# Performance work log

Hardware: AMD Instinct MI355X
Metric: run time of the kernel (lower is better)

## Reference

```python
import jax, jax.numpy as jnp
import numpy as np

D_IN = 1024
D_OUT = 1024
NUM_HEADS = 16
HEAD_DIM = D_OUT // NUM_HEADS


def setup_inputs() -> dict:
    key = jax.random.key(0)
    ks = jax.random.split(key, 6)
    B, T = 2, 2048
    x = jax.random.normal(ks[0], (B, T, D_IN), dtype=jnp.float32)
    s = 1.0 / np.sqrt(D_IN)
    Wq = jax.random.normal(ks[1], (D_IN, D_OUT), dtype=jnp.float32) * s
    Wk = jax.random.normal(ks[2], (D_IN, D_OUT), dtype=jnp.float32) * s
    Wv = jax.random.normal(ks[3], (D_IN, D_OUT), dtype=jnp.float32) * s
    Wo = jax.random.normal(ks[4], (D_OUT, D_OUT), dtype=jnp.float32) * (1.0 / np.sqrt(D_OUT))
    bo = jnp.zeros((D_OUT,), dtype=jnp.float32)
    return {"x": x, "Wq": Wq, "Wk": Wk, "Wv": Wv, "Wo": Wo, "bo": bo}


def reference(x, Wq, Wk, Wv, Wo, bo):
    B, T, _ = x.shape
    # project and split heads -> (B, H, T, Dh)
    def split(t):
        return t.reshape(B, T, NUM_HEADS, HEAD_DIM).transpose(0, 2, 1, 3)
    Q = split(x @ Wq)
    K = split(x @ Wk)
    V = split(x @ Wv)
    scale = HEAD_DIM ** -0.5
    scores = jnp.einsum('bhqd,bhkd->bhqk', Q, K) * scale  # (B,H,T,T)
    causal = jnp.triu(jnp.ones((T, T), dtype=bool), k=1)
    scores = jnp.where(causal, -jnp.inf, scores)
    weights = jax.nn.softmax(scores, axis=-1)
    ctx = jnp.einsum('bhqk,bhkd->bhqd', weights, V)  # (B,H,T,Dh)
    ctx = ctx.transpose(0, 2, 1, 3).reshape(B, T, D_OUT)
    return ctx @ Wo + bo
```

## Files before the change

kernel.cpp:

```cpp
#include <hip/hip_runtime.h>
#include <hip/hip_bf16.h>

#define NH   16
#define HD   64
#define BB   2
#define TT   2048
#define DIN  1024
#define DOUT 1024
#define MTOT (BB*TT)

#define QSCALE 0.18033688011112042f
#define MAXC   20.0f

typedef __hip_bfloat16 bf16;
typedef short bf16x8  __attribute__((ext_vector_type(8)));
typedef float f32x4   __attribute__((ext_vector_type(4)));
typedef float f32x16  __attribute__((ext_vector_type(16)));

__device__ __forceinline__ bf16 f2bf(float f){ return __float2bfloat16(f); }

__device__ __forceinline__ void gld16(const bf16* g, bf16* l){
    __builtin_amdgcn_global_load_lds(
        (const __attribute__((address_space(1))) unsigned int*)g,
        (__attribute__((address_space(3))) unsigned int*)l,
        16, 0, 0);
}

__device__ __forceinline__ size_t qk_off(int bh, int t, int d){
    return (size_t)bh*131072 + (size_t)(((t>>5)*4 + (d>>4))*512)
         + ((t&31) + 32*((d>>3)&1))*8 + (d&7);
}
__device__ __forceinline__ size_t v_off(int bh, int t, int d){
    return (size_t)bh*131072 + (size_t)((((t>>4)*2) + (d>>5))*512)
         + ((d&31) + 32*((t>>2)&1))*8 + ((t&3) + 4*((t>>3)&1));
}

__global__ void prep_cast_x(const float* __restrict__ x, bf16* __restrict__ xb){
    int i = blockIdx.x*blockDim.x + threadIdx.x;
    float4 v = ((const float4*)x)[i];
    bf16 o[4] = {f2bf(v.x), f2bf(v.y), f2bf(v.z), f2bf(v.w)};
    *(ushort4*)&xb[(size_t)i*4] = *(ushort4*)o;
}

__global__ void prep_weights(const float* __restrict__ Wq, const float* __restrict__ Wk,
                             const float* __restrict__ Wv, const float* __restrict__ Wo,
                             bf16* __restrict__ WT){
    __shared__ float tile[64][65];
    const int n0 = blockIdx.y*64, k0 = blockIdx.x*64;
    const float* W;
    switch (n0 >> 10){ case 0: W=Wq; break; case 1: W=Wk; break; case 2: W=Wv; break; default: W=Wo; }
    const int c0 = n0 & 1023;
    const int tr = threadIdx.x >> 6;
    const int tc = threadIdx.x & 63;
    #pragma unroll
    for (int it = 0; it < 16; it++){
        int k = k0 + it*4 + tr;
        tile[it*4 + tr][tc] = W[(size_t)k*DOUT + c0 + tc];
    }
    __syncthreads();
    #pragma unroll
    for (int it = 0; it < 16; it++){
        int n = it*4 + tr;
        WT[(size_t)(n0 + n)*DIN + k0 + tc] = f2bf(tile[tc][n]);
    }
}

__launch_bounds__(256)
__global__ void gemm_qkv(const bf16* __restrict__ Xb, const bf16* __restrict__ WT,
                         bf16* __restrict__ Qf, bf16* __restrict__ Kf, bf16* __restrict__ Vf){
    __shared__ __align__(16) bf16 As[128*32];
    __shared__ __align__(16) bf16 Bs[128*32];
    const int n0 = blockIdx.x * 128;
    const int m0 = blockIdx.y * 128;
    const int tid = threadIdx.x;
    const int wave = tid >> 6, lane = tid & 63;
    const int wm = (wave & 1) * 64, wn = (wave >> 1) * 64;
    const int quad = lane >> 4, l16 = lane & 15;
    const int arow = wave*16 + (lane >> 2);
    const int acol = (lane & 3) * 8;

    f32x4 acc[4][4] = {};
    for (int k0 = 0; k0 < DIN; k0 += 32){
        #pragma unroll
        for (int j = 0; j < 2; j++){
            int r = arow + j*64;
            gld16(&Xb[(size_t)(m0 + r)*DIN + k0 + acol], &As[r*32 + acol]);
            gld16(&WT[(size_t)(n0 + r)*DIN + k0 + acol], &Bs[r*32 + acol]);
        }
        __syncthreads();
        bf16x8 af[4], bfr[4];
        #pragma unroll
        for (int mi = 0; mi < 4; mi++) af[mi]  = *(bf16x8*)&As[(wm + mi*16 + l16)*32 + quad*8];
        #pragma unroll
        for (int ni = 0; ni < 4; ni++) bfr[ni] = *(bf16x8*)&Bs[(wn + ni*16 + l16)*32 + quad*8];
        #pragma unroll
        for (int mi = 0; mi < 4; mi++)
            #pragma unroll
            for (int ni = 0; ni < 4; ni++)
                acc[mi][ni] = __builtin_amdgcn_mfma_f32_16x16x32_bf16(af[mi], bfr[ni], acc[mi][ni], 0, 0, 0);
        __syncthreads();
    }
    #pragma unroll
    for (int mi = 0; mi < 4; mi++){
        #pragma unroll
        for (int ni = 0; ni < 4; ni++){
            int col = n0 + wn + ni*16 + l16;
            int which = col >> 10;
            int c = col & 1023;
            int h = c >> 6, d = c & 63;
            int m_base = m0 + wm + mi*16 + quad*4;
            int b = m_base >> 11, t0 = m_base & 2047;
            int bh = b*NH + h;
            if (which == 2){
                bf16 pk[4];
                #pragma unroll
                for (int r = 0; r < 4; r++) pk[r] = f2bf(acc[mi][ni][r]);
                *(ushort4*)&Vf[v_off(bh, t0, d)] = *(ushort4*)pk;
            } else if (which == 0){
                #pragma unroll
                for (int r = 0; r < 4; r++)
                    Qf[qk_off(bh, t0 + r, d)] = f2bf(acc[mi][ni][r] * QSCALE);
            } else {
                #pragma unroll
                for (int r = 0; r < 4; r++)
                    Kf[qk_off(bh, t0 + r, d)] = f2bf(acc[mi][ni][r]);
            }
        }
    }
}

__launch_bounds__(256, 4)
__global__ void attn(const bf16* __restrict__ Qf, const bf16* __restrict__ Kf,
                     const bf16* __restrict__ Vf, bf16* __restrict__ ctx){
    __shared__ float Lo[2*64*36];
    __shared__ float Ls[2*64];
    const int blk  = blockIdx.x;
    const int bh   = (blk & 7) + 8*((blk >> 3) & 3);
    const int g    = blk >> 5;
    const int wave = threadIdx.x >> 6, lane = threadIdx.x & 63;
    const int pair = wave >> 1, half = wave & 1;
    const int qb   = pair ? g : (63 - g);
    const int nh   = (qb + 1) >> 1;
    const int tstart = half ? nh : 0;
    const int tend   = half ? qb : (nh - 1);
    const int h32  = lane >> 5, l32 = lane & 31;
    const int b    = bh >> 4, head = bh & 15;
    const bf16* Qb = Qf + (size_t)bh*131072 + lane*8;
    const bf16* Kb = Kf + (size_t)bh*131072 + lane*8;
    const bf16* Vb = Vf + (size_t)bh*131072 + lane*8;

    bf16x8 qf[4];
    #pragma unroll
    for (int ks = 0; ks < 4; ks++)
        qf[ks] = *(const bf16x8*)(Qb + (qb*4 + ks)*512);

    bf16x8 kc[4], vc[4];
    #pragma unroll
    for (int i = 0; i < 4; i++){
        kc[i] = *(const bf16x8*)(Kb + (tstart*4 + i)*512);
        vc[i] = *(const bf16x8*)(Vb + (tstart*4 + i)*512);
    }

    f32x16 o0 = {}, o1 = {};
    float lsum = 0.f;

    for (int tb = tstart; tb <= tend; tb++){
        f32x16 s = {};
        #pragma unroll
        for (int ks = 0; ks < 4; ks++)
            s = __builtin_amdgcn_mfma_f32_32x32x16_bf16(kc[ks], qf[ks], s, 0, 0, 0);
        if (tb < tend){
            #pragma unroll
            for (int i = 0; i < 4; i++)
                kc[i] = *(const bf16x8*)(Kb + ((tb+1)*4 + i)*512);
        }
        if (tb == qb){
            #pragma unroll
            for (int r = 0; r < 16; r++){
                int trow = (r&3) + 8*(r>>2) + 4*h32;
                if (trow > l32) s[r] = -1e30f;
            }
        }
        float p[16];
        #pragma unroll
        for (int r = 0; r < 16; r++){
            p[r] = __builtin_amdgcn_exp2f(s[r] - MAXC);
            lsum += p[r];
        }
        #pragma unroll
        for (int ki = 0; ki < 2; ki++){
            bf16 pb[8];
            #pragma unroll
            for (int j = 0; j < 8; j++) pb[j] = f2bf(p[ki*8 + j]);
            bf16x8 pbv = *(bf16x8*)pb;
            o0 = __builtin_amdgcn_mfma_f32_32x32x16_bf16(vc[ki*2+0], pbv, o0, 0, 0, 0);
            o1 = __builtin_amdgcn_mfma_f32_32x32x16_bf16(vc[ki*2+1], pbv, o1, 0, 0, 0);
        }
        if (tb < tend){
            #pragma unroll
            for (int i = 0; i < 4; i++)
                vc[i] = *(const bf16x8*)(Vb + ((tb+1)*4 + i)*512);
        }
    }

    if (half){
        float* lo = &Lo[pair*64*36 + lane*36];
        #pragma unroll
        for (int c = 0; c < 4; c++){
            f32x4 w4 = { o0[c*4+0], o0[c*4+1], o0[c*4+2], o0[c*4+3] };
            *(f32x4*)&lo[c*4] = w4;
        }
        #pragma unroll
        for (int c = 0; c < 4; c++){
            f32x4 w4 = { o1[c*4+0], o1[c*4+1], o1[c*4+2], o1[c*4+3] };
            *(f32x4*)&lo[16 + c*4] = w4;
        }
        Ls[pair*64 + lane] = lsum;
    }
    __syncthreads();
    if (!half){
        const float* lo = &Lo[pair*64*36 + lane*36];
        #pragma unroll
        for (int c = 0; c < 4; c++){
            f32x4 r4 = *(const f32x4*)&lo[c*4];
            #pragma unroll
            for (int i = 0; i < 4; i++) o0[c*4+i] += r4[i];
        }
        #pragma unroll
        for (int c = 0; c < 4; c++){
            f32x4 r4 = *(const f32x4*)&lo[16 + c*4];
            #pragma unroll
            for (int i = 0; i < 4; i++) o1[c*4+i] += r4[i];
        }
        float lc  = lsum + Ls[pair*64 + lane];
        float lq  = lc + __shfl_xor(lc, 32);
        float inv = 1.0f / lq;
        const int q = qb*32 + l32;
        bf16* cp = ctx + ((size_t)(b*TT + q))*DOUT + head*HD;
        #pragma unroll
        for (int db = 0; db < 2; db++){
            #pragma unroll
            for (int rq = 0; rq < 4; rq++){
                bf16 pk[4];
                #pragma unroll
                for (int i = 0; i < 4; i++){
                    float ov = (db ? o1[rq*4 + i] : o0[rq*4 + i]) * inv;
                    pk[i] = f2bf(ov);
                }
                int d0 = db*32 + rq*8 + h32*4;
                *(ushort4*)&cp[d0] = *(ushort4*)pk;
            }
        }
    }
}

__launch_bounds__(256)
__global__ void gemm_out(const bf16* __restrict__ Cx, const bf16* __restrict__ WoT,
                         const float* __restrict__ bo, float* __restrict__ out){
    __shared__ __align__(16) bf16 As[128*32];
    __shared__ __align__(16) bf16 Bs[128*32];
    const int n0 = blockIdx.x * 128;
    const int m0 = blockIdx.y * 128;
    const int tid = threadIdx.x;
    const int wave = tid >> 6, lane = tid & 63;
    const int wm = (wave & 1) * 64, wn = (wave >> 1) * 64;
    const int quad = lane >> 4, l16 = lane & 15;
    const int arow = wave*16 + (lane >> 2);
    const int acol = (lane & 3) * 8;

    f32x4 acc[4][4] = {};
    for (int k0 = 0; k0 < DOUT; k0 += 32){
        #pragma unroll
        for (int j = 0; j < 2; j++){
            int r = arow + j*64;
            gld16(&Cx[(size_t)(m0 + r)*DOUT + k0 + acol],  &As[r*32 + acol]);
            gld16(&WoT[(size_t)(n0 + r)*DOUT + k0 + acol], &Bs[r*32 + acol]);
        }
        __syncthreads();
        bf16x8 af[4], bfr[4];
        #pragma unroll
        for (int mi = 0; mi < 4; mi++) af[mi]  = *(bf16x8*)&As[(wm + mi*16 + l16)*32 + quad*8];
        #pragma unroll
        for (int ni = 0; ni < 4; ni++) bfr[ni] = *(bf16x8*)&Bs[(wn + ni*16 + l16)*32 + quad*8];
        #pragma unroll
        for (int mi = 0; mi < 4; mi++)
            #pragma unroll
            for (int ni = 0; ni < 4; ni++)
                acc[mi][ni] = __builtin_amdgcn_mfma_f32_16x16x32_bf16(af[mi], bfr[ni], acc[mi][ni], 0, 0, 0);
        __syncthreads();
    }
    #pragma unroll
    for (int mi = 0; mi < 4; mi++){
        #pragma unroll
        for (int ni = 0; ni < 4; ni++){
            int n = n0 + wn + ni*16 + l16;
            float bias = bo[n];
            #pragma unroll
            for (int r = 0; r < 4; r++){
                int m = m0 + wm + mi*16 + quad*4 + r;
                out[(size_t)m*DOUT + n] = acc[mi][ni][r] + bias;
            }
        }
    }
}

extern "C" void kernel_launch(void* const* d_in, const int* in_sizes, int n_in,
                              void* d_out, int out_size, void* d_ws, size_t ws_size,
                              hipStream_t stream){
    const float* x  = (const float*)d_in[0];
    const float* Wq = (const float*)d_in[1];
    const float* Wk = (const float*)d_in[2];
    const float* Wv = (const float*)d_in[3];
    const float* Wo = (const float*)d_in[4];
    const float* bo = (const float*)d_in[5];
    float* out = (float*)d_out;

    char* ws = (char*)d_ws;
    bf16* xb  = (bf16*)(ws);
    bf16* WT  = (bf16*)(ws + ((size_t)8  << 20));
    bf16* Qf  = (bf16*)(ws + ((size_t)16 << 20));
    bf16* Kf  = (bf16*)(ws + ((size_t)24 << 20));
    bf16* Vf  = (bf16*)(ws + ((size_t)32 << 20));
    bf16* ctx = (bf16*)(ws + ((size_t)40 << 20));
    bf16* WoT = WT + (size_t)3072*DIN;

    prep_cast_x <<<dim3(MTOT*DIN/4/256), 256, 0, stream>>>(x, xb);
    prep_weights<<<dim3(16, 64),          256, 0, stream>>>(Wq, Wk, Wv, Wo, WT);
    gemm_qkv    <<<dim3(24, 32),          256, 0, stream>>>(xb, WT, Qf, Kf, Vf);
    attn        <<<dim3(1024),            256, 0, stream>>>(Qf, Kf, Vf, ctx);
    gemm_out    <<<dim3(8, 32),           256, 0, stream>>>(ctx, WoT, bo, out);
}
```

Measured before the change: 175.7 us.

## Merge prep kernels, use swizzled K=64 GEMM tiles, split attention KV across four waves

```diff
diff --git a/kernel.cpp b/kernel.cpp
--- a/kernel.cpp
+++ b/kernel.cpp
@@ -35,18 +35,21 @@
          + ((d&31) + 32*((t>>2)&1))*8 + ((t&3) + 4*((t>>3)&1));
 }
 
-__global__ void prep_cast_x(const float* __restrict__ x, bf16* __restrict__ xb){
-    int i = blockIdx.x*blockDim.x + threadIdx.x;
-    float4 v = ((const float4*)x)[i];
-    bf16 o[4] = {f2bf(v.x), f2bf(v.y), f2bf(v.z), f2bf(v.w)};
-    *(ushort4*)&xb[(size_t)i*4] = *(ushort4*)o;
-}
-
-__global__ void prep_weights(const float* __restrict__ Wq, const float* __restrict__ Wk,
-                             const float* __restrict__ Wv, const float* __restrict__ Wo,
-                             bf16* __restrict__ WT){
+__global__ void prep_all(const float* __restrict__ x,
+                         const float* __restrict__ Wq, const float* __restrict__ Wk,
+                         const float* __restrict__ Wv, const float* __restrict__ Wo,
+                         bf16* __restrict__ xb, bf16* __restrict__ WT){
     __shared__ float tile[64][65];
-    const int n0 = blockIdx.y*64, k0 = blockIdx.x*64;
+    const int blk = blockIdx.x;
+    if (blk < 4096){
+        int i = blk*256 + threadIdx.x;
+        float4 v = ((const float4*)x)[i];
+        bf16 o[4] = {f2bf(v.x), f2bf(v.y), f2bf(v.z), f2bf(v.w)};
+        *(ushort4*)&xb[(size_t)i*4] = *(ushort4*)o;
+        return;
+    }
+    const int wb = blk - 4096;
+    const int n0 = (wb >> 4) * 64, k0 = (wb & 15) * 64;
     const float* W;
     switch (n0 >> 10){ case 0: W=Wq; break; case 1: W=Wk; break; case 2: W=Wv; break; default: W=Wo; }
     const int c0 = n0 & 1023;
@@ -68,36 +71,46 @@
 __launch_bounds__(256)
 __global__ void gemm_qkv(const bf16* __restrict__ Xb, const bf16* __restrict__ WT,
                          bf16* __restrict__ Qf, bf16* __restrict__ Kf, bf16* __restrict__ Vf){
-    __shared__ __align__(16) bf16 As[128*32];
-    __shared__ __align__(16) bf16 Bs[128*32];
+    __shared__ __align__(16) bf16 As[128*64];
+    __shared__ __align__(16) bf16 Bs[128*64];
     const int n0 = blockIdx.x * 128;
     const int m0 = blockIdx.y * 128;
     const int tid = threadIdx.x;
     const int wave = tid >> 6, lane = tid & 63;
     const int wm = (wave & 1) * 64, wn = (wave >> 1) * 64;
     const int quad = lane >> 4, l16 = lane & 15;
-    const int arow = wave*16 + (lane >> 2);
-    const int acol = (lane & 3) * 8;
+    const int srow = wave*8 + (lane >> 3);
+    const int schk = lane & 7;
 
     f32x4 acc[4][4] = {};
-    for (int k0 = 0; k0 < DIN; k0 += 32){
-        #pragma unroll
-        for (int j = 0; j < 2; j++){
-            int r = arow + j*64;
-            gld16(&Xb[(size_t)(m0 + r)*DIN + k0 + acol], &As[r*32 + acol]);
-            gld16(&WT[(size_t)(n0 + r)*DIN + k0 + acol], &Bs[r*32 + acol]);
+    for (int k0 = 0; k0 < DIN; k0 += 64){
+        #pragma unroll
+        for (int j = 0; j < 4; j++){
+            int r = srow + j*32;
+            int gc = (schk ^ (r & 7)) << 3;
+            gld16(&Xb[(size_t)(m0 + r)*DIN + k0 + gc], &As[r*64 + schk*8]);
+            gld16(&WT[(size_t)(n0 + r)*DIN + k0 + gc], &Bs[r*64 + schk*8]);
         }
         __syncthreads();
-        bf16x8 af[4], bfr[4];
-        #pragma unroll
-        for (int mi = 0; mi < 4; mi++) af[mi]  = *(bf16x8*)&As[(wm + mi*16 + l16)*32 + quad*8];
-        #pragma unroll
-        for (int ni = 0; ni < 4; ni++) bfr[ni] = *(bf16x8*)&Bs[(wn + ni*16 + l16)*32 + quad*8];
-        #pragma unroll
-        for (int mi = 0; mi < 4; mi++)
-            #pragma unroll
-            for (int ni = 0; ni < 4; ni++)
-                acc[mi][ni] = __builtin_amdgcn_mfma_f32_16x16x32_bf16(af[mi], bfr[ni], acc[mi][ni], 0, 0, 0);
+        #pragma unroll
+        for (int ks = 0; ks < 2; ks++){
+            bf16x8 af[4], bfr[4];
+            #pragma unroll
+            for (int mi = 0; mi < 4; mi++){
+                int row = wm + mi*16 + l16;
+                af[mi] = *(bf16x8*)&As[row*64 + (((ks*4 + quad) ^ (row & 7)) << 3)];
+            }
+            #pragma unroll
+            for (int ni = 0; ni < 4; ni++){
+                int row = wn + ni*16 + l16;
+                bfr[ni] = *(bf16x8*)&Bs[row*64 + (((ks*4 + quad) ^ (row & 7)) << 3)];
+            }
+            #pragma unroll
+            for (int mi = 0; mi < 4; mi++)
+                #pragma unroll
+                for (int ni = 0; ni < 4; ni++)
+                    acc[mi][ni] = __builtin_amdgcn_mfma_f32_16x16x32_bf16(af[mi], bfr[ni], acc[mi][ni], 0, 0, 0);
+        }
         __syncthreads();
     }
     #pragma unroll
@@ -132,17 +145,15 @@
 __launch_bounds__(256, 4)
 __global__ void attn(const bf16* __restrict__ Qf, const bf16* __restrict__ Kf,
                      const bf16* __restrict__ Vf, bf16* __restrict__ ctx){
-    __shared__ float Lo[2*64*36];
-    __shared__ float Ls[2*64];
+    __shared__ float Lo[3*64*36];
+    __shared__ float Ls[3*64];
     const int blk  = blockIdx.x;
     const int bh   = (blk & 7) + 8*((blk >> 3) & 3);
-    const int g    = blk >> 5;
+    const int qb   = 63 - (blk >> 5);
     const int wave = threadIdx.x >> 6, lane = threadIdx.x & 63;
-    const int pair = wave >> 1, half = wave & 1;
-    const int qb   = pair ? g : (63 - g);
-    const int nh   = (qb + 1) >> 1;
-    const int tstart = half ? nh : 0;
-    const int tend   = half ? qb : (nh - 1);
+    const int n    = qb + 1;
+    const int tstart = (n*wave) >> 2;
+    const int tend   = ((n*(wave+1)) >> 2) - 1;
     const int h32  = lane >> 5, l32 = lane & 31;
     const int b    = bh >> 4, head = bh & 15;
     const bf16* Qb = Qf + (size_t)bh*131072 + lane*8;
@@ -203,8 +214,8 @@
         }
     }
 
-    if (half){
-        float* lo = &Lo[pair*64*36 + lane*36];
+    if (wave != 0){
+        float* lo = &Lo[(wave-1)*2304 + lane*36];
         #pragma unroll
         for (int c = 0; c < 4; c++){
             f32x4 w4 = { o0[c*4+0], o0[c*4+1], o0[c*4+2], o0[c*4+3] };
@@ -215,24 +226,28 @@
             f32x4 w4 = { o1[c*4+0], o1[c*4+1], o1[c*4+2], o1[c*4+3] };
             *(f32x4*)&lo[16 + c*4] = w4;
         }
-        Ls[pair*64 + lane] = lsum;
+        Ls[(wave-1)*64 + lane] = lsum;
     }
     __syncthreads();
-    if (!half){
-        const float* lo = &Lo[pair*64*36 + lane*36];
-        #pragma unroll
-        for (int c = 0; c < 4; c++){
-            f32x4 r4 = *(const f32x4*)&lo[c*4];
-            #pragma unroll
-            for (int i = 0; i < 4; i++) o0[c*4+i] += r4[i];
-        }
-        #pragma unroll
-        for (int c = 0; c < 4; c++){
-            f32x4 r4 = *(const f32x4*)&lo[16 + c*4];
-            #pragma unroll
-            for (int i = 0; i < 4; i++) o1[c*4+i] += r4[i];
-        }
-        float lc  = lsum + Ls[pair*64 + lane];
+    if (wave == 0){
+        float lc = lsum;
+        #pragma unroll
+        for (int w = 0; w < 3; w++){
+            const float* lo = &Lo[w*2304 + lane*36];
+            #pragma unroll
+            for (int c = 0; c < 4; c++){
+                f32x4 r4 = *(const f32x4*)&lo[c*4];
+                #pragma unroll
+                for (int i = 0; i < 4; i++) o0[c*4+i] += r4[i];
+            }
+            #pragma unroll
+            for (int c = 0; c < 4; c++){
+                f32x4 r4 = *(const f32x4*)&lo[16 + c*4];
+                #pragma unroll
+                for (int i = 0; i < 4; i++) o1[c*4+i] += r4[i];
+            }
+            lc += Ls[w*64 + lane];
+        }
         float lq  = lc + __shfl_xor(lc, 32);
         float inv = 1.0f / lq;
         const int q = qb*32 + l32;
@@ -257,48 +272,63 @@
 __launch_bounds__(256)
 __global__ void gemm_out(const bf16* __restrict__ Cx, const bf16* __restrict__ WoT,
                          const float* __restrict__ bo, float* __restrict__ out){
-    __shared__ __align__(16) bf16 As[128*32];
-    __shared__ __align__(16) bf16 Bs[128*32];
-    const int n0 = blockIdx.x * 128;
+    __shared__ __align__(16) bf16 As[128*64];
+    __shared__ __align__(16) bf16 Bs[64*64];
+    const int n0 = blockIdx.x * 64;
     const int m0 = blockIdx.y * 128;
     const int tid = threadIdx.x;
     const int wave = tid >> 6, lane = tid & 63;
-    const int wm = (wave & 1) * 64, wn = (wave >> 1) * 64;
+    const int wm = (wave & 1) * 64, wn = (wave >> 1) * 32;
     const int quad = lane >> 4, l16 = lane & 15;
-    const int arow = wave*16 + (lane >> 2);
-    const int acol = (lane & 3) * 8;
-
-    f32x4 acc[4][4] = {};
-    for (int k0 = 0; k0 < DOUT; k0 += 32){
+    const int srow = wave*8 + (lane >> 3);
+    const int schk = lane & 7;
+
+    f32x4 acc[4][2] = {};
+    for (int k0 = 0; k0 < DOUT; k0 += 64){
+        #pragma unroll
+        for (int j = 0; j < 4; j++){
+            int r = srow + j*32;
+            int gc = (schk ^ (r & 7)) << 3;
+            gld16(&Cx[(size_t)(m0 + r)*DOUT + k0 + gc], &As[r*64 + schk*8]);
+        }
         #pragma unroll
         for (int j = 0; j < 2; j++){
-            int r = arow + j*64;
-            gld16(&Cx[(size_t)(m0 + r)*DOUT + k0 + acol],  &As[r*32 + acol]);
-            gld16(&WoT[(size_t)(n0 + r)*DOUT + k0 + acol], &Bs[r*32 + acol]);
+            int r = srow + j*32;
+            int gc = (schk ^ (r & 7)) << 3;
+            gld16(&WoT[(size_t)(n0 + r)*DOUT + k0 + gc], &Bs[r*64 + schk*8]);
         }
         __syncthreads();
-        bf16x8 af[4], bfr[4];
-        #pragma unroll
-        for (int mi = 0; mi < 4; mi++) af[mi]  = *(bf16x8*)&As[(wm + mi*16 + l16)*32 + quad*8];
-        #pragma unroll
-        for (int ni = 0; ni < 4; ni++) bfr[ni] = *(bf16x8*)&Bs[(wn + ni*16 + l16)*32 + quad*8];
-        #pragma unroll
-        for (int mi = 0; mi < 4; mi++)
-            #pragma unroll
-            for (int ni = 0; ni < 4; ni++)
-                acc[mi][ni] = __builtin_amdgcn_mfma_f32_16x16x32_bf16(af[mi], bfr[ni], acc[mi][ni], 0, 0, 0);
+        #pragma unroll
+        for (int ks = 0; ks < 2; ks++){
+            bf16x8 af[4], bfr[2];
+            #pragma unroll
+            for (int mi = 0; mi < 4; mi++){
+                int row = wm + mi*16 + l16;
+                af[mi] = *(bf16x8*)&As[row*64 + (((ks*4 + quad) ^ (row & 7)) << 3)];
+            }
+            #pragma unroll
+            for (int ni = 0; ni < 2; ni++){
+                int row = wn + ni*16 + l16;
+                bfr[ni] = *(bf16x8*)&Bs[row*64 + (((ks*4 + quad) ^ (row & 7)) << 3)];
+            }
+            #pragma unroll
+            for (int mi = 0; mi < 4; mi++)
+                #pragma unroll
+                for (int ni = 0; ni < 2; ni++)
+                    acc[mi][ni] = __builtin_amdgcn_mfma_f32_16x16x32_bf16(af[mi], bfr[ni], acc[mi][ni], 0, 0, 0);
+        }
         __syncthreads();
     }
     #pragma unroll
     for (int mi = 0; mi < 4; mi++){
         #pragma unroll
-        for (int ni = 0; ni < 4; ni++){
-            int n = n0 + wn + ni*16 + l16;
-            float bias = bo[n];
+        for (int ni = 0; ni < 2; ni++){
+            int nn = n0 + wn + ni*16 + l16;
+            float bias = bo[nn];
             #pragma unroll
             for (int r = 0; r < 4; r++){
                 int m = m0 + wm + mi*16 + quad*4 + r;
-                out[(size_t)m*DOUT + n] = acc[mi][ni][r] + bias;
+                out[(size_t)m*DOUT + nn] = acc[mi][ni][r] + bias;
             }
         }
     }
@@ -324,9 +354,8 @@
     bf16* ctx = (bf16*)(ws + ((size_t)40 << 20));
     bf16* WoT = WT + (size_t)3072*DIN;
 
-    prep_cast_x <<<dim3(MTOT*DIN/4/256), 256, 0, stream>>>(x, xb);
-    prep_weights<<<dim3(16, 64),          256, 0, stream>>>(Wq, Wk, Wv, Wo, WT);
-    gemm_qkv    <<<dim3(24, 32),          256, 0, stream>>>(xb, WT, Qf, Kf, Vf);
-    attn        <<<dim3(1024),            256, 0, stream>>>(Qf, Kf, Vf, ctx);
-    gemm_out    <<<dim3(8, 32),           256, 0, stream>>>(ctx, WoT, bo, out);
-}
+    prep_all <<<dim3(5120),    256, 0, stream>>>(x, Wq, Wk, Wv, Wo, xb, WT);
+    gemm_qkv <<<dim3(24, 32),  256, 0, stream>>>(xb, WT, Qf, Kf, Vf);
+    attn     <<<dim3(2048),    256, 0, stream>>>(Qf, Kf, Vf, ctx);
+    gemm_out <<<dim3(16, 32),  256, 0, stream>>>(ctx, WoT, bo, out);
+}
```

Measured after the change: 172.8 us. Within noise of the previous version (-1.6%).
